# Kernel tuning notes

Measured on AMD Instinct MI355X. Metric: run time of the kernel, lower is better.

Reference implementation:

```python
import jax, jax.numpy as jnp
import numpy as np

B, H, W, C, M1, M2, NL = 16, 41, 40, 48, 12, 12, 4
EPS = 1e-5
TX = jnp.linspace(0.0, 2.0 * np.pi, H, dtype=jnp.float32)      # theta grid, len 41
TY = jnp.linspace(0.0, 15.0, W, dtype=jnp.float32)             # z grid, len 40
DTX = 2.0 * np.pi / (H - 1)
DTY = 15.0 / (W - 1)
LAM1 = (2j * np.pi) * jnp.fft.fftfreq(H, d=DTX).astype(jnp.float32)  # [H] complex64
LAM2 = (2j * np.pi) * jnp.fft.fftfreq(W, d=DTY).astype(jnp.float32)  # [W] complex64


def setup_inputs() -> dict:
    key = jax.random.key(0)
    k = jax.random.split(key, 10)
    scale = 1.0 / (C * C)
    u = lambda kk, s: scale * jax.random.uniform(kk, s, dtype=jnp.float32)
    n = lambda kk, s, sc: sc * jax.random.normal(kk, s, dtype=jnp.float32)
    return {
        "x": n(k[0], (B, H, W, 1), 1.0),
        "fc0_w": n(k[1], (C, 3), 0.3), "fc0_b": jnp.zeros((C,), jnp.float32),
        "poles1": u(k[2], (NL, C, C, M1, 2)),          # real/imag split of cfloat params
        "poles2": u(k[3], (NL, C, C, M2, 2)),
        "residues": u(k[4], (NL, C, C, M1, M2, 2)),
        "conv_w": n(k[5], (NL, C, C), 1.0 / np.sqrt(C)), "conv_b": jnp.zeros((NL, C), jnp.float32),
        "fc1_w": n(k[6], (128, C), 1.0 / np.sqrt(C)), "fc1_b": jnp.zeros((128,), jnp.float32),
        "fc2_w": n(k[7], (2, 128), 1.0 / np.sqrt(128)), "fc2_b": jnp.zeros((2,), jnp.float32),
    }


def _cplx(a):
    return a[..., 0] + 1j * a[..., 1]


def _inorm(h):  # InstanceNorm2d(affine=False): per-(b,c) over H,W, biased var
    m = h.mean(axis=(-2, -1), keepdims=True)
    v = h.var(axis=(-2, -1), keepdims=True)
    return (h - m) / jnp.sqrt(v + EPS)


def _pr2d(h, p1ri, p2ri, resri):
    # h: [B,C,H,W] real. Pole-residue Laplace spectral operator (PR2d.forward).
    p1 = _cplx(p1ri)     # [Ci,Co,M1]
    p2 = _cplx(p2ri)     # [Ci,Co,M2]
    res = _cplx(resri)   # [Ci,Co,M1,M2]
    alpha = jnp.fft.fft2(h, axes=(-2, -1))                      # [B,Ci,H,W] complex
    inv1 = 1.0 / (LAM1[None, None, None, :] - p1[..., None])    # [Ci,Co,M1,H]
    inv2 = 1.0 / (LAM2[None, None, None, :] - p2[..., None])    # [Ci,Co,M2,W]
    # output_residue1[b,k,o,x] = sum_{i,p,q} alpha * res * inv1 * inv2
    S = jnp.einsum('ikpq,ikpo,ikqx->ikox', res, inv1, inv2)     # [Ci,Co,H,W]
    res1 = jnp.einsum('biox,ikox->bkox', alpha, S)              # [B,Co,H,W]
    # output_residue2[b,k,p,q] = sum_{i,o,x} alpha * res * inv1 * inv2
    A = jnp.einsum('biox,ikpo->bikpx', alpha, inv1)             # [B,Ci,Co,M1,W]
    G = jnp.einsum('bikpx,ikqx->bikpq', A, inv2)                # [B,Ci,Co,M1,M2]
    r2 = jnp.einsum('bikpq,ikpq->bkpq', G, res)                 # [B,Co,M1,M2]
    x1 = jnp.fft.ifft2(res1, axes=(-2, -1)).real
    # reconstruction: exp(pole * t) outer products (term1/term2/term3 in torch)
    E1 = jnp.exp(p1[..., None] * TX[None, None, None, :])       # [Ci,Co,M1,H]
    E2 = jnp.exp(p2[..., None] * TY[None, None, None, :])       # [Ci,Co,M2,W]
    U = jnp.einsum('kbpq,bipz->kbiqz', r2, E1)                  # [B,Ci,Co,M2,H]
    x2 = jnp.einsum('kbiqz,biqx->kizx', U, E2).real / (H * W)   # [B,Co,H,W]
    return x1 + x2


def reference(x, fc0_w, fc0_b, poles1, poles2, residues, conv_w, conv_b,
              fc1_w, fc1_b, fc2_w, fc2_b):
    b = x.shape[0]
    gx = jnp.broadcast_to(jnp.linspace(0.0, 1.0, H, dtype=jnp.float32)[None, :, None, None], (b, H, W, 1))
    gy = jnp.broadcast_to(jnp.linspace(0.0, 1.0, W, dtype=jnp.float32)[None, None, :, None], (b, H, W, 1))
    h = jnp.concatenate([x, gx, gy], axis=-1)                   # [B,H,W,3]
    h = jnp.einsum('bhwi,ci->bhwc', h, fc0_w) + fc0_b           # fc0
    h = jnp.transpose(h, (0, 3, 1, 2))                          # [B,C,H,W]
    for l in range(NL):
        x1 = _inorm(_pr2d(_inorm(h), poles1[l], poles2[l], residues[l]))
        x2 = jnp.einsum('oi,bihw->bohw', conv_w[l], h) + conv_b[l][None, :, None, None]
        h = jnp.sin(x1 + x2)
    h = jnp.transpose(h, (0, 2, 3, 1))                          # [B,H,W,C]
    h = jnp.sin(jnp.einsum('bhwc,oc->bhwo', h, fc1_w) + fc1_b)
    out = jnp.einsum('bhwc,oc->bhwo', h, fc2_w) + fc2_b         # [B,H,W,2]
    return out
```

## Files before the change

kernel.cpp:

```cpp
#include <hip/hip_runtime.h>
#include <math.h>

#define DI __device__ __forceinline__

constexpr int B = 16, H = 41, W = 40, C = 48, M1 = 12, M2 = 12, NL = 4;
constexpr int HW = H * W;
constexpr float EPS = 1e-5f;
constexpr float PI_F = 3.14159265358979323846f;

__device__ float  g_h[2][B * C * HW];
__device__ float2 g_alpha[B * C * HW];
__device__ float2 g_inv1t[NL][C * C][H * 16];
__device__ float2 g_inv2a[NL][C * C][M2 * W];
__device__ float2 g_E1a[NL][C * C][M1 * H];
__device__ float2 g_E2a[NL][C * C][M2 * W];
__device__ float2 g_Sa[NL][C * C][HW];
__device__ float2 g_res1[B * C * HW];
__device__ float  g_x1[B * C * HW];
__device__ float2 g_r2[B * C * M1 * M2];
__device__ float2 g_Zr[C * C][B * M1 * M2];
__device__ float  g_xpart[3][B * C][HW];
__device__ float  g_mu[B * C];
__device__ float  g_rstd[B * C];
__device__ float2 g_wfh[H * H];
__device__ float2 g_wfw[W * W];

DI float2 cmadd(float2 a, float2 b, float2 acc) {
    acc.x = fmaf(a.x, b.x, fmaf(-a.y, b.y, acc.x));
    acc.y = fmaf(a.x, b.y, fmaf(a.y, b.x, acc.y));
    return acc;
}
DI float2 cmul(float2 a, float2 b) {
    return make_float2(a.x * b.x - a.y * b.y, a.x * b.y + a.y * b.x);
}

__global__ void k_tw() {
    int tid = blockIdx.x * 256 + threadIdx.x;
    if (tid < H * H) {
        int o = tid / H, h = tid % H;
        float ph = -2.0f * PI_F * (float)((o * h) % H) / (float)H;
        float s, c; sincosf(ph, &s, &c);
        g_wfh[tid] = make_float2(c, s);
    }
    int t2 = tid - H * H;
    if (t2 >= 0 && t2 < W * W) {
        int o = t2 / W, w = t2 % W;
        float ph = -2.0f * PI_F * (float)((o * w) % W) / (float)W;
        float s, c; sincosf(ph, &s, &c);
        g_wfw[t2] = make_float2(c, s);
    }
}

__global__ void k_fc0(const float* __restrict__ x, const float* __restrict__ w,
                      const float* __restrict__ bias) {
    int idx = blockIdx.x * 256 + threadIdx.x;
    if (idx >= B * C * HW) return;
    int hw = idx % HW; int bc = idx / HW; int c = bc % C; int b = bc / C;
    int hh = hw / W, ww = hw % W;
    float xv = x[b * HW + hw];
    float gx = hh * (1.0f / (H - 1));
    float gy = ww * (1.0f / (W - 1));
    g_h[0][idx] = fmaf(w[c * 3 + 0], xv, fmaf(w[c * 3 + 1], gx, fmaf(w[c * 3 + 2], gy, bias[c])));
}

__global__ __launch_bounds__(256) void k_fft(int src) {
    int bid = blockIdx.x;
    const float* hp = &g_h[src][(size_t)bid * HW];
    __shared__ float sh[HW];
    __shared__ float2 st[HW];
    __shared__ float2 swf[H * H];
    __shared__ float red[8];
    int tid = threadIdx.x;
    float s = 0.f, ss = 0.f;
    for (int i = tid; i < HW; i += 256) { float v = hp[i]; sh[i] = v; s += v; ss += v * v; }
    for (int i = tid; i < H * H; i += 256) swf[i] = g_wfh[i];
    for (int off = 32; off; off >>= 1) { s += __shfl_down(s, off); ss += __shfl_down(ss, off); }
    if ((tid & 63) == 0) { red[tid >> 6] = s; red[4 + (tid >> 6)] = ss; }
    __syncthreads();
    if (tid == 0) {
        float S = red[0] + red[1] + red[2] + red[3];
        float SS = red[4] + red[5] + red[6] + red[7];
        float mean = S * (1.0f / HW);
        float var = SS * (1.0f / HW) - mean * mean;
        red[0] = mean; red[1] = rsqrtf(var + EPS);
    }
    __syncthreads();
    float mean = red[0], rstd = red[1];
    for (int i = tid; i < HW; i += 256) sh[i] = (sh[i] - mean) * rstd;
    __syncthreads();
    for (int i = tid; i < 21 * W; i += 256) {
        int o0 = (i / W) * 2, w = i % W;
        bool pair = (o0 + 1) < H;
        float2 a0 = make_float2(0.f, 0.f), a1 = make_float2(0.f, 0.f);
        for (int h = 0; h < H; h++) {
            float v = sh[h * W + w];
            float2 t0 = swf[o0 * H + h];
            a0.x = fmaf(t0.x, v, a0.x); a0.y = fmaf(t0.y, v, a0.y);
            if (pair) {
                float2 t1 = swf[o0 * H + H + h];
                a1.x = fmaf(t1.x, v, a1.x); a1.y = fmaf(t1.y, v, a1.y);
            }
        }
        st[o0 * W + w] = a0;
        if (pair) st[(o0 + 1) * W + w] = a1;
    }
    __syncthreads();
    for (int t = tid; t < W * W; t += 256) {
        int x = t / W, w = t % W;
        swf[x * 41 + w] = g_wfw[t];
    }
    __syncthreads();
    float2* ap = &g_alpha[(size_t)bid * HW];
    for (int i = tid; i < H * 20; i += 256) {
        int o = i / 20, x0 = (i % 20) * 2;
        float2 a0 = make_float2(0.f, 0.f), a1 = make_float2(0.f, 0.f);
        for (int w = 0; w < W; w++) {
            float2 sv = st[o * W + w];
            a0 = cmadd(sv, swf[x0 * 41 + w], a0);
            a1 = cmadd(sv, swf[(x0 + 1) * 41 + w], a1);
        }
        ap[o * W + x0] = a0;
        ap[o * W + x0 + 1] = a1;
    }
}

__global__ __launch_bounds__(256) void k_tbS(const float* __restrict__ p1, const float* __restrict__ p2,
                                             const float* __restrict__ res_in) {
    int gb = blockIdx.x;
    int l = gb / (C * C), pk = gb % (C * C);
    int tid = threadIdx.x;
    __shared__ float2 sinv1[M1 * H];
    __shared__ float2 sinv2[M2 * W];
    __shared__ float2 sT[M1 * W];
    __shared__ float2 sres[M1 * M2];
    const float* pp1 = p1 + (size_t)gb * M1 * 2;
    const float* pp2 = p2 + (size_t)gb * M2 * 2;
    for (int t = tid; t < M1 * H; t += 256) {
        int p = t / H, o = t % H;
        float pr = pp1[p * 2], pi = pp1[p * 2 + 1];
        int ko = (o <= H / 2) ? o : o - H;
        float lam = (40.0f / 41.0f) * (float)ko;
        float a = -pr, b = lam - pi;
        float d = 1.0f / (a * a + b * b);
        float2 inv = make_float2(a * d, -b * d);
        sinv1[t] = inv;
        float tt = o * (2.0f * PI_F / (H - 1));
        float er = expf(pr * tt);
        float sn, cs; sincosf(pi * tt, &sn, &cs);
        g_E1a[l][pk][t] = make_float2(er * cs, er * sn);
    }
    for (int t = tid; t < M2 * W; t += 256) {
        int q = t / W, x = t % W;
        float pr = pp2[q * 2], pi = pp2[q * 2 + 1];
        int kx = (x < W / 2) ? x : x - W;
        float lam = (2.0f * PI_F * 39.0f / 600.0f) * (float)kx;
        float a = -pr, b = lam - pi;
        float d = 1.0f / (a * a + b * b);
        float2 inv = make_float2(a * d, -b * d);
        sinv2[t] = inv;
        g_inv2a[l][pk][t] = inv;
        float tt = x * (15.0f / (W - 1));
        float er = expf(pr * tt);
        float sn, cs; sincosf(pi * tt, &sn, &cs);
        g_E2a[l][pk][t] = make_float2(er * cs, er * sn);
    }
    const float2* rp = (const float2*)res_in + (size_t)gb * M1 * M2;
    for (int t = tid; t < M1 * M2; t += 256) sres[t] = rp[t];
    __syncthreads();
    for (int t = tid; t < H * 16; t += 256) {
        int o = t >> 4, p = t & 15;
        g_inv1t[l][pk][t] = (p < M1) ? sinv1[p * H + o] : make_float2(0.f, 0.f);
    }
    for (int t = tid; t < M1 * W; t += 256) {
        int p = t / W, x = t % W;
        float2 acc = make_float2(0.f, 0.f);
        for (int q = 0; q < M2; q++) acc = cmadd(sres[p * M2 + q], sinv2[q * W + x], acc);
        sT[t] = acc;
    }
    __syncthreads();
    float2* sp = g_Sa[l][pk];
    for (int t = tid; t < HW; t += 256) {
        int o = t / W, x = t % W;
        float2 acc = make_float2(0.f, 0.f);
        for (int p = 0; p < M1; p++) acc = cmadd(sinv1[p * H + o], sT[p * W + x], acc);
        sp[t] = acc;
    }
}

__global__ __launch_bounds__(256) void k_res1(int l) {
    int bid = blockIdx.x;
    int ch = bid % 7;
    int rest = bid / 7;
    int kq = rest % 12, bp = rest / 12;
    int hw = ch * 256 + threadIdx.x;
    if (hw >= HW) return;
    int b0 = bp * 2, k0 = kq * 4;
    float2 acc[2][4];
#pragma unroll
    for (int u = 0; u < 2; u++)
#pragma unroll
        for (int v = 0; v < 4; v++) acc[u][v] = make_float2(0.f, 0.f);
    for (int i = 0; i < C; i++) {
        float2 a0 = g_alpha[(size_t)((b0    ) * C + i) * HW + hw];
        float2 a1 = g_alpha[(size_t)((b0 + 1) * C + i) * HW + hw];
        float2 s0 = g_Sa[l][i * C + k0][hw];
        float2 s1 = g_Sa[l][i * C + k0 + 1][hw];
        float2 s2 = g_Sa[l][i * C + k0 + 2][hw];
        float2 s3 = g_Sa[l][i * C + k0 + 3][hw];
        acc[0][0] = cmadd(a0, s0, acc[0][0]);
        acc[0][1] = cmadd(a0, s1, acc[0][1]);
        acc[0][2] = cmadd(a0, s2, acc[0][2]);
        acc[0][3] = cmadd(a0, s3, acc[0][3]);
        acc[1][0] = cmadd(a1, s0, acc[1][0]);
        acc[1][1] = cmadd(a1, s1, acc[1][1]);
        acc[1][2] = cmadd(a1, s2, acc[1][2]);
        acc[1][3] = cmadd(a1, s3, acc[1][3]);
    }
#pragma unroll
    for (int u = 0; u < 2; u++)
#pragma unroll
        for (int v = 0; v < 4; v++)
            g_res1[(size_t)((b0 + u) * C + k0 + v) * HW + hw] = acc[u][v];
}

__global__ __launch_bounds__(256) void k_ifftfin() {
    int bid = blockIdx.x; int tid = threadIdx.x;
    __shared__ float2 s0[HW], s1[HW];
    __shared__ float2 swf[H * H];
    __shared__ float red[8];
    const float2* rp = &g_res1[(size_t)bid * HW];
    for (int i = tid; i < HW; i += 256) s0[i] = rp[i];
    for (int i = tid; i < H * H; i += 256) swf[i] = g_wfh[i];
    __syncthreads();
    for (int i = tid; i < 21 * W; i += 256) {
        int h0 = (i / W) * 2, x = i % W;
        bool pair = (h0 + 1) < H;
        float2 a0 = make_float2(0.f, 0.f), a1 = make_float2(0.f, 0.f);
        for (int o = 0; o < H; o++) {
            float2 v = s0[o * W + x];
            float2 t0 = swf[o * H + h0];
            a0.x = fmaf(v.x, t0.x, fmaf(v.y, t0.y, a0.x));
            a0.y = fmaf(v.y, t0.x, fmaf(-v.x, t0.y, a0.y));
            if (pair) {
                float2 t1 = swf[o * H + h0 + 1];
                a1.x = fmaf(v.x, t1.x, fmaf(v.y, t1.y, a1.x));
                a1.y = fmaf(v.y, t1.x, fmaf(-v.x, t1.y, a1.y));
            }
        }
        s1[h0 * W + x] = a0;
        if (pair) s1[(h0 + 1) * W + x] = a1;
    }
    __syncthreads();
    for (int t = tid; t < W * W; t += 256) {
        int x = t / W, w = t % W;
        swf[x * 41 + w] = g_wfw[t];
    }
    __syncthreads();
    float* xp = &g_x1[(size_t)bid * HW];
    const float* q0p = &g_xpart[0][bid][0];
    const float* q1p = &g_xpart[1][bid][0];
    const float* q2p = &g_xpart[2][bid][0];
    float s = 0.f, ss = 0.f;
    for (int i = tid; i < H * 20; i += 256) {
        int h = i / 20, w0 = (i % 20) * 2;
        float a0 = 0.f, a1 = 0.f;
        for (int x = 0; x < W; x++) {
            float2 v = s1[h * W + x];
            float2 t0 = swf[x * 41 + w0];
            float2 t1 = swf[x * 41 + w0 + 1];
            a0 = fmaf(v.x, t0.x, fmaf(v.y, t0.y, a0));
            a1 = fmaf(v.x, t1.x, fmaf(v.y, t1.y, a1));
        }
        int id0 = h * W + w0;
        float v0 = (a0 + q0p[id0] + q1p[id0] + q2p[id0]) * (1.0f / (H * W));
        float v1 = (a1 + q0p[id0 + 1] + q1p[id0 + 1] + q2p[id0 + 1]) * (1.0f / (H * W));
        xp[id0] = v0; xp[id0 + 1] = v1;
        s += v0 + v1; ss += v0 * v0 + v1 * v1;
    }
    for (int off = 32; off; off >>= 1) { s += __shfl_down(s, off); ss += __shfl_down(ss, off); }
    if ((tid & 63) == 0) { red[tid >> 6] = s; red[4 + (tid >> 6)] = ss; }
    __syncthreads();
    if (tid == 0) {
        float S = red[0] + red[1] + red[2] + red[3];
        float SS = red[4] + red[5] + red[6] + red[7];
        float mean = S * (1.0f / HW);
        float var = SS * (1.0f / HW) - mean * mean;
        g_mu[bid] = mean; g_rstd[bid] = rsqrtf(var + EPS);
    }
}

__global__ __launch_bounds__(320) void k_r2a(const float* __restrict__ res_in, int l) {
    int bid = blockIdx.x;
    int xcd = bid & 7, idx = bid >> 3;
    int i = (idx / (C * 4)) * 8 + xcd;
    int rem = idx % (C * 4);
    int k = rem >> 2;
    int bc = rem & 3;
    int pk = i * C + k;
    int tid = threadIdx.x;
    __shared__ float2 sY[4 * M1 * 41];
    __shared__ float2 si1t[H * 16];
    __shared__ float2 si2[M2 * 41];
    __shared__ float2 sres[M1 * M2];
    for (int t = tid; t < H * 16; t += 320) si1t[t] = g_inv1t[l][pk][t];
    for (int t = tid; t < M2 * W; t += 320) {
        int q = t / W, x = t % W;
        si2[q * 41 + x] = g_inv2a[l][pk][t];
    }
    const float2* rp = (const float2*)res_in + (size_t)(l * C * C + pk) * M1 * M2;
    for (int t = tid; t < M1 * M2; t += 320) sres[t] = rp[t];
    __syncthreads();
    {
        int ph = tid / 160;
        int r2t = tid % 160;
        int bloc = r2t / 40, x = r2t % 40;
        int b = bc * 4 + bloc;
        int p0 = ph * 6;
        const float2* ap = &g_alpha[(size_t)(b * C + i) * HW + x];
        float2 yacc[6];
#pragma unroll
        for (int p = 0; p < 6; p++) yacc[p] = make_float2(0.f, 0.f);
        for (int o = 0; o < H; o++) {
            float2 a = ap[o * W];
            const float4* e4 = (const float4*)&si1t[o * 16 + p0];
#pragma unroll
            for (int j = 0; j < 3; j++) {
                float4 ee = e4[j];
                yacc[2 * j]     = cmadd(make_float2(ee.x, ee.y), a, yacc[2 * j]);
                yacc[2 * j + 1] = cmadd(make_float2(ee.z, ee.w), a, yacc[2 * j + 1]);
            }
        }
#pragma unroll
        for (int p = 0; p < 6; p++) sY[(bloc * M1 + p0 + p) * 41 + x] = yacc[p];
    }
    __syncthreads();
    if (tid < 288) {
        int bloc = tid / 72, rem2 = tid % 72;
        int p = rem2 / 6, qh = rem2 % 6;
        int q0 = qh * 2;
        float2 zacc0 = make_float2(0.f, 0.f), zacc1 = make_float2(0.f, 0.f);
        const float2* yrow = &sY[(bloc * M1 + p) * 41];
        const float2* s2a = &si2[q0 * 41];
        const float2* s2b = &si2[(q0 + 1) * 41];
        for (int x = 0; x < W; x++) {
            float2 y = yrow[x];
            zacc0 = cmadd(y, s2a[x], zacc0);
            zacc1 = cmadd(y, s2b[x], zacc1);
        }
        int b = bc * 4 + bloc;
        float2* out = &g_Zr[pk][b * (M1 * M2) + p * M2 + q0];
        out[0] = cmul(sres[p * M2 + q0], zacc0);
        out[1] = cmul(sres[p * M2 + q0 + 1], zacc1);
    }
}

__global__ __launch_bounds__(256) void k_r2b() {
    int t = blockIdx.x * 256 + threadIdx.x;
    if (t >= B * C * M1 * M2) return;
    int pq = t % (M1 * M2);
    int k = (t / (M1 * M2)) % C;
    int b = t / (M1 * M2 * C);
    float2 acc = make_float2(0.f, 0.f);
    for (int i = 0; i < C; i++) {
        float2 v = g_Zr[i * C + k][b * (M1 * M2) + pq];
        acc.x += v.x; acc.y += v.y;
    }
    g_r2[(size_t)(b * C + k) * (M1 * M2) + pq] = acc;
}

constexpr int XNCI = 2;
__global__ __launch_bounds__(256) void k_x2p(int l) {
    int bid = blockIdx.x;
    int xcd = bid & 7, rest = bid >> 3;
    int part = rest % 3;
    int idx = rest / 3;
    int k = (idx / B) * 8 + xcd;
    int b = idx % B;
    int tid = threadIdx.x;
    __shared__ float2 sE1[XNCI * M1 * 44];
    __shared__ float2 sV [XNCI * M1 * 40];
    __shared__ float2 sE2[XNCI * M2 * 41];
    __shared__ float2 sr2[XNCI * M1 * M2];
    int xh = tid % 20, zq = tid / 20;
    int x0 = xh * 2, z0 = zq * 4;
    float accr[4][2];
#pragma unroll
    for (int zi = 0; zi < 4; zi++) { accr[zi][0] = 0.f; accr[zi][1] = 0.f; }

    int cg0 = part * (C / XNCI / 3);
    for (int cg = cg0; cg < cg0 + C / XNCI / 3; cg++) {
        for (int t = tid; t < XNCI * M1 * 44; t += 256) {
            int j = t / (M1 * 44), rem = t % (M1 * 44);
            int p = rem / 44, z = rem % 44;
            sE1[t] = (z < H) ? g_E1a[l][(cg * XNCI + j) * C + k][p * H + z]
                             : make_float2(0.f, 0.f);
        }
        for (int t = tid; t < XNCI * M2 * W; t += 256) {
            int j = t / (M2 * W), rem = t % (M2 * W);
            sE2[(t / W) * 41 + (t % W)] = g_E2a[l][(cg * XNCI + j) * C + k][rem];
        }
        for (int t = tid; t < XNCI * M1 * M2; t += 256) {
            int j = t / (M1 * M2);
            sr2[t] = g_r2[(size_t)(b * C + cg * XNCI + j) * (M1 * M2) + (t % (M1 * M2))];
        }
        __syncthreads();
        for (int r = 0; r < 2; r++) {
            int id = tid + r * 256;
            if (id < XNCI * 6 * W) {
                int j = id / (6 * W), rem = id % (6 * W);
                int pp = rem / W, x = rem % W;
                int p0 = pp * 2;
                float2 a0 = make_float2(0.f, 0.f), a1 = make_float2(0.f, 0.f);
#pragma unroll
                for (int q = 0; q < M2; q++) {
                    float2 e = sE2[(j * M2 + q) * 41 + x];
                    a0 = cmadd(sr2[j * (M1 * M2) + p0 * M2 + q], e, a0);
                    a1 = cmadd(sr2[j * (M1 * M2) + (p0 + 1) * M2 + q], e, a1);
                }
                sV[(j * M1 + p0) * 40 + x] = a0;
                sV[(j * M1 + p0 + 1) * 40 + x] = a1;
            }
        }
        __syncthreads();
        if (tid < 240 && z0 < H) {
            for (int jp = 0; jp < XNCI * M1; jp++) {
                float4 v  = *(const float4*)&sV[jp * 40 + x0];
                float4 eA = *(const float4*)&sE1[jp * 44 + z0];
                float4 eB = *(const float4*)&sE1[jp * 44 + z0 + 2];
                accr[0][0] = fmaf(eA.x, v.x, fmaf(-eA.y, v.y, accr[0][0]));
                accr[0][1] = fmaf(eA.x, v.z, fmaf(-eA.y, v.w, accr[0][1]));
                accr[1][0] = fmaf(eA.z, v.x, fmaf(-eA.w, v.y, accr[1][0]));
                accr[1][1] = fmaf(eA.z, v.z, fmaf(-eA.w, v.w, accr[1][1]));
                accr[2][0] = fmaf(eB.x, v.x, fmaf(-eB.y, v.y, accr[2][0]));
                accr[2][1] = fmaf(eB.x, v.z, fmaf(-eB.y, v.w, accr[2][1]));
                accr[3][0] = fmaf(eB.z, v.x, fmaf(-eB.w, v.y, accr[3][0]));
                accr[3][1] = fmaf(eB.z, v.z, fmaf(-eB.w, v.w, accr[3][1]));
            }
        }
        __syncthreads();
    }
    float* op = &g_xpart[part][b * C + k][0];
    if (tid < 240 && z0 < H) {
#pragma unroll
        for (int zi = 0; zi < 4; zi++) {
            int z = z0 + zi;
            if (z < H) { op[z * W + x0] = accr[zi][0]; op[z * W + x0 + 1] = accr[zi][1]; }
        }
    }
}

constexpr int TILE = 128;
constexpr int NTILE = (HW + TILE - 1) / TILE;
__global__ __launch_bounds__(256) void k_comb(const float* __restrict__ cw,
                                              const float* __restrict__ cb, int l, int src) {
    int b = blockIdx.x / NTILE;
    int t0 = (blockIdx.x % NTILE) * TILE;
    int tid = threadIdx.x;
    __shared__ float shh[C * TILE];
    __shared__ float scw[C * C];
    __shared__ float smu[C], srs[C], scb[C];
    for (int i = tid; i < C * C; i += 256) scw[i] = cw[l * C * C + i];
    for (int i = tid; i < C; i += 256) {
        smu[i] = g_mu[b * C + i]; srs[i] = g_rstd[b * C + i]; scb[i] = cb[l * C + i];
    }
    for (int i = tid; i < C * TILE; i += 256) {
        int c = i / TILE, t = i % TILE; int hw = t0 + t;
        shh[i] = (hw < HW) ? g_h[src][(size_t)(b * C + c) * HW + hw] : 0.f;
    }
    __syncthreads();
    for (int i = tid; i < C * TILE; i += 256) {
        int o = i / TILE, t = i % TILE; int hw = t0 + t;
        if (hw >= HW) continue;
        float acc = scb[o];
        for (int ci = 0; ci < C; ci++) acc = fmaf(scw[o * C + ci], shh[ci * TILE + t], acc);
        float prn = (g_x1[(size_t)(b * C + o) * HW + hw] - smu[o]) * srs[o];
        g_h[src ^ 1][(size_t)(b * C + o) * HW + hw] = sinf(prn + acc);
    }
}

__global__ __launch_bounds__(256) void k_head(const float* __restrict__ w1, const float* __restrict__ b1,
                                              const float* __restrict__ w2, const float* __restrict__ b2,
                                              float* __restrict__ out, int src) {
    __shared__ float sw1[128 * C];
    __shared__ float sb1[128], sw2[2 * 128];
    int tid = threadIdx.x;
    for (int i = tid; i < 128 * C; i += 256) sw1[i] = w1[i];
    for (int i = tid; i < 128; i += 256) sb1[i] = b1[i];
    for (int i = tid; i < 256; i += 256) sw2[i] = w2[i];
    __syncthreads();
    int pt = blockIdx.x * 256 + tid;
    if (pt >= B * HW) return;
    int b = pt / HW, hw = pt % HW;
    float hv[C];
#pragma unroll
    for (int c = 0; c < C; c++) hv[c] = g_h[src][(size_t)(b * C + c) * HW + hw];
    float o0 = b2[0], o1 = b2[1];
    for (int j = 0; j < 128; j++) {
        float a = sb1[j];
#pragma unroll
        for (int c = 0; c < C; c++) a = fmaf(sw1[j * C + c], hv[c], a);
        float sv = sinf(a);
        o0 = fmaf(sw2[j], sv, o0);
        o1 = fmaf(sw2[128 + j], sv, o1);
    }
    out[pt * 2 + 0] = o0; out[pt * 2 + 1] = o1;
}

extern "C" void kernel_launch(void* const* d_in, const int* in_sizes, int n_in,
                              void* d_out, int out_size, void* d_ws, size_t ws_size,
                              hipStream_t stream) {
    const float* x    = (const float*)d_in[0];
    const float* fc0w = (const float*)d_in[1];
    const float* fc0b = (const float*)d_in[2];
    const float* p1   = (const float*)d_in[3];
    const float* p2   = (const float*)d_in[4];
    const float* res  = (const float*)d_in[5];
    const float* cw   = (const float*)d_in[6];
    const float* cb   = (const float*)d_in[7];
    const float* w1   = (const float*)d_in[8];
    const float* b1   = (const float*)d_in[9];
    const float* w2   = (const float*)d_in[10];
    const float* b2   = (const float*)d_in[11];
    float* out = (float*)d_out;

    k_tw<<<(H * H + W * W + 255) / 256, 256, 0, stream>>>();
    k_fc0<<<(B * C * HW + 255) / 256, 256, 0, stream>>>(x, fc0w, fc0b);
    k_tbS<<<NL * C * C, 256, 0, stream>>>(p1, p2, res);
    int src = 0;
    for (int l = 0; l < NL; l++) {
        k_fft<<<B * C, 256, 0, stream>>>(src);
        k_res1<<<672, 256, 0, stream>>>(l);
        k_r2a<<<C * C * 4, 320, 0, stream>>>(res, l);
        k_r2b<<<(B * C * M1 * M2 + 255) / 256, 256, 0, stream>>>();
        k_x2p<<<3 * B * C, 256, 0, stream>>>(l);
        k_ifftfin<<<B * C, 256, 0, stream>>>();
        k_comb<<<B * NTILE, 256, 0, stream>>>(cw, cb, l, src);
        src ^= 1;
    }
    k_head<<<(B * HW + 255) / 256, 256, 0, stream>>>(w1, b1, w2, b2, out, src);
}
```

Baseline: 1.779 ms.

## Register-block FFT and inverse-FFT DFT loops and split x2p over six parts

The DFT matmul loops in the forward FFT and the inverse-FFT/finalise kernels now have each thread compute a 2x4 output tile, using float4 shared-memory loads and reusing each twiddle and data value across several accumulators. The twiddle stride is padded to 42 so the vector loads stay aligned. Separately, the x2p channel reduction is split six ways instead of three, which doubles the block count and the number of partial buffers summed in the finalise step. This cuts shared-memory traffic and adds parallelism, at the cost of only 210 of 256 threads being active in those loops and extra partial-sum memory traffic.

Result: faster. 1.696 ms (-4.7%).

```diff
diff --git a/kernel.cpp b/kernel.cpp
--- a/kernel.cpp
+++ b/kernel.cpp
@@ -5,6 +5,7 @@
 
 constexpr int B = 16, H = 41, W = 40, C = 48, M1 = 12, M2 = 12, NL = 4;
 constexpr int HW = H * W;
+constexpr int NPART = 6;
 constexpr float EPS = 1e-5f;
 constexpr float PI_F = 3.14159265358979323846f;
 
@@ -19,7 +20,7 @@
 __device__ float  g_x1[B * C * HW];
 __device__ float2 g_r2[B * C * M1 * M2];
 __device__ float2 g_Zr[C * C][B * M1 * M2];
-__device__ float  g_xpart[3][B * C][HW];
+__device__ float  g_xpart[NPART][B * C][HW];
 __device__ float  g_mu[B * C];
 __device__ float  g_rstd[B * C];
 __device__ float2 g_wfh[H * H];
@@ -66,9 +67,9 @@
 __global__ __launch_bounds__(256) void k_fft(int src) {
     int bid = blockIdx.x;
     const float* hp = &g_h[src][(size_t)bid * HW];
-    __shared__ float sh[HW];
-    __shared__ float2 st[HW];
-    __shared__ float2 swf[H * H];
+    __shared__ __align__(16) float sh[HW];
+    __shared__ __align__(16) float2 st[HW];
+    __shared__ __align__(16) float2 swf[H * H];
     __shared__ float red[8];
     int tid = threadIdx.x;
     float s = 0.f, ss = 0.f;
@@ -88,21 +89,33 @@
     float mean = red[0], rstd = red[1];
     for (int i = tid; i < HW; i += 256) sh[i] = (sh[i] - mean) * rstd;
     __syncthreads();
-    for (int i = tid; i < 21 * W; i += 256) {
-        int o0 = (i / W) * 2, w = i % W;
+    if (tid < 210) {
+        int op = tid / 10, wq = tid % 10;
+        int o0 = op * 2, w0 = wq * 4;
         bool pair = (o0 + 1) < H;
-        float2 a0 = make_float2(0.f, 0.f), a1 = make_float2(0.f, 0.f);
+        int o1 = pair ? o0 + 1 : o0;
+        float2 a0[4], a1[4];
+#pragma unroll
+        for (int j = 0; j < 4; j++) { a0[j] = make_float2(0.f, 0.f); a1[j] = make_float2(0.f, 0.f); }
         for (int h = 0; h < H; h++) {
-            float v = sh[h * W + w];
+            float4 v = *(const float4*)&sh[h * W + w0];
             float2 t0 = swf[o0 * H + h];
-            a0.x = fmaf(t0.x, v, a0.x); a0.y = fmaf(t0.y, v, a0.y);
-            if (pair) {
-                float2 t1 = swf[o0 * H + H + h];
-                a1.x = fmaf(t1.x, v, a1.x); a1.y = fmaf(t1.y, v, a1.y);
-            }
-        }
-        st[o0 * W + w] = a0;
-        if (pair) st[(o0 + 1) * W + w] = a1;
+            float2 t1 = swf[o1 * H + h];
+            a0[0].x = fmaf(t0.x, v.x, a0[0].x); a0[0].y = fmaf(t0.y, v.x, a0[0].y);
+            a0[1].x = fmaf(t0.x, v.y, a0[1].x); a0[1].y = fmaf(t0.y, v.y, a0[1].y);
+            a0[2].x = fmaf(t0.x, v.z, a0[2].x); a0[2].y = fmaf(t0.y, v.z, a0[2].y);
+            a0[3].x = fmaf(t0.x, v.w, a0[3].x); a0[3].y = fmaf(t0.y, v.w, a0[3].y);
+            a1[0].x = fmaf(t1.x, v.x, a1[0].x); a1[0].y = fmaf(t1.y, v.x, a1[0].y);
+            a1[1].x = fmaf(t1.x, v.y, a1[1].x); a1[1].y = fmaf(t1.y, v.y, a1[1].y);
+            a1[2].x = fmaf(t1.x, v.z, a1[2].x); a1[2].y = fmaf(t1.y, v.z, a1[2].y);
+            a1[3].x = fmaf(t1.x, v.w, a1[3].x); a1[3].y = fmaf(t1.y, v.w, a1[3].y);
+        }
+#pragma unroll
+        for (int j = 0; j < 4; j++) st[o0 * W + w0 + j] = a0[j];
+        if (pair) {
+#pragma unroll
+            for (int j = 0; j < 4; j++) st[o1 * W + w0 + j] = a1[j];
+        }
     }
     __syncthreads();
     for (int t = tid; t < W * W; t += 256) {
@@ -111,16 +124,30 @@
     }
     __syncthreads();
     float2* ap = &g_alpha[(size_t)bid * HW];
-    for (int i = tid; i < H * 20; i += 256) {
-        int o = i / 20, x0 = (i % 20) * 2;
-        float2 a0 = make_float2(0.f, 0.f), a1 = make_float2(0.f, 0.f);
+    if (tid < 210) {
+        int op = tid / 10, xq = tid % 10;
+        int o0 = op * 2, x0 = xq * 4;
+        bool pair = (o0 + 1) < H;
+        int o1 = pair ? o0 + 1 : o0;
+        float2 c0[4], c1[4];
+#pragma unroll
+        for (int j = 0; j < 4; j++) { c0[j] = make_float2(0.f, 0.f); c1[j] = make_float2(0.f, 0.f); }
         for (int w = 0; w < W; w++) {
-            float2 sv = st[o * W + w];
-            a0 = cmadd(sv, swf[x0 * 41 + w], a0);
-            a1 = cmadd(sv, swf[(x0 + 1) * 41 + w], a1);
-        }
-        ap[o * W + x0] = a0;
-        ap[o * W + x0 + 1] = a1;
+            float2 s0v = st[o0 * W + w];
+            float2 s1v = st[o1 * W + w];
+#pragma unroll
+            for (int j = 0; j < 4; j++) {
+                float2 e = swf[(x0 + j) * 41 + w];
+                c0[j] = cmadd(s0v, e, c0[j]);
+                c1[j] = cmadd(s1v, e, c1[j]);
+            }
+        }
+#pragma unroll
+        for (int j = 0; j < 4; j++) ap[o0 * W + x0 + j] = c0[j];
+        if (pair) {
+#pragma unroll
+            for (int j = 0; j < 4; j++) ap[o1 * W + x0 + j] = c1[j];
+        }
     }
 }
 
@@ -225,57 +252,110 @@
 
 __global__ __launch_bounds__(256) void k_ifftfin() {
     int bid = blockIdx.x; int tid = threadIdx.x;
-    __shared__ float2 s0[HW], s1[HW];
-    __shared__ float2 swf[H * H];
+    __shared__ __align__(16) float2 s0[HW], s1[HW];
+    __shared__ __align__(16) float2 swf[H * H];
     __shared__ float red[8];
     const float2* rp = &g_res1[(size_t)bid * HW];
     for (int i = tid; i < HW; i += 256) s0[i] = rp[i];
     for (int i = tid; i < H * H; i += 256) swf[i] = g_wfh[i];
     __syncthreads();
-    for (int i = tid; i < 21 * W; i += 256) {
-        int h0 = (i / W) * 2, x = i % W;
+    if (tid < 210) {
+        int hp = tid / 10, xq = tid % 10;
+        int h0 = hp * 2, x0 = xq * 4;
         bool pair = (h0 + 1) < H;
-        float2 a0 = make_float2(0.f, 0.f), a1 = make_float2(0.f, 0.f);
+        int h1 = pair ? h0 + 1 : h0;
+        float2 a0[4], a1[4];
+#pragma unroll
+        for (int j = 0; j < 4; j++) { a0[j] = make_float2(0.f, 0.f); a1[j] = make_float2(0.f, 0.f); }
         for (int o = 0; o < H; o++) {
-            float2 v = s0[o * W + x];
+            float4 v01 = *(const float4*)&s0[o * W + x0];
+            float4 v23 = *(const float4*)&s0[o * W + x0 + 2];
             float2 t0 = swf[o * H + h0];
-            a0.x = fmaf(v.x, t0.x, fmaf(v.y, t0.y, a0.x));
-            a0.y = fmaf(v.y, t0.x, fmaf(-v.x, t0.y, a0.y));
-            if (pair) {
-                float2 t1 = swf[o * H + h0 + 1];
-                a1.x = fmaf(v.x, t1.x, fmaf(v.y, t1.y, a1.x));
-                a1.y = fmaf(v.y, t1.x, fmaf(-v.x, t1.y, a1.y));
-            }
-        }
-        s1[h0 * W + x] = a0;
-        if (pair) s1[(h0 + 1) * W + x] = a1;
+            float2 t1 = swf[o * H + h1];
+            a0[0].x = fmaf(v01.x, t0.x, fmaf(v01.y, t0.y, a0[0].x));
+            a0[0].y = fmaf(v01.y, t0.x, fmaf(-v01.x, t0.y, a0[0].y));
+            a0[1].x = fmaf(v01.z, t0.x, fmaf(v01.w, t0.y, a0[1].x));
+            a0[1].y = fmaf(v01.w, t0.x, fmaf(-v01.z, t0.y, a0[1].y));
+            a0[2].x = fmaf(v23.x, t0.x, fmaf(v23.y, t0.y, a0[2].x));
+            a0[2].y = fmaf(v23.y, t0.x, fmaf(-v23.x, t0.y, a0[2].y));
+            a0[3].x = fmaf(v23.z, t0.x, fmaf(v23.w, t0.y, a0[3].x));
+            a0[3].y = fmaf(v23.w, t0.x, fmaf(-v23.z, t0.y, a0[3].y));
+            a1[0].x = fmaf(v01.x, t1.x, fmaf(v01.y, t1.y, a1[0].x));
+            a1[0].y = fmaf(v01.y, t1.x, fmaf(-v01.x, t1.y, a1[0].y));
+            a1[1].x = fmaf(v01.z, t1.x, fmaf(v01.w, t1.y, a1[1].x));
+            a1[1].y = fmaf(v01.w, t1.x, fmaf(-v01.z, t1.y, a1[1].y));
+            a1[2].x = fmaf(v23.x, t1.x, fmaf(v23.y, t1.y, a1[2].x));
+            a1[2].y = fmaf(v23.y, t1.x, fmaf(-v23.x, t1.y, a1[2].y));
+            a1[3].x = fmaf(v23.z, t1.x, fmaf(v23.w, t1.y, a1[3].x));
+            a1[3].y = fmaf(v23.w, t1.x, fmaf(-v23.z, t1.y, a1[3].y));
+        }
+#pragma unroll
+        for (int j = 0; j < 4; j++) s1[h0 * W + x0 + j] = a0[j];
+        if (pair) {
+#pragma unroll
+            for (int j = 0; j < 4; j++) s1[h1 * W + x0 + j] = a1[j];
+        }
     }
     __syncthreads();
     for (int t = tid; t < W * W; t += 256) {
         int x = t / W, w = t % W;
-        swf[x * 41 + w] = g_wfw[t];
+        swf[x * 42 + w] = g_wfw[t];
     }
     __syncthreads();
     float* xp = &g_x1[(size_t)bid * HW];
-    const float* q0p = &g_xpart[0][bid][0];
-    const float* q1p = &g_xpart[1][bid][0];
-    const float* q2p = &g_xpart[2][bid][0];
     float s = 0.f, ss = 0.f;
-    for (int i = tid; i < H * 20; i += 256) {
-        int h = i / 20, w0 = (i % 20) * 2;
-        float a0 = 0.f, a1 = 0.f;
+    if (tid < 210) {
+        int hp = tid / 10, wq = tid % 10;
+        int h0 = hp * 2, w0 = wq * 4;
+        bool pair = (h0 + 1) < H;
+        int h1 = pair ? h0 + 1 : h0;
+        float acc0[4] = {0.f, 0.f, 0.f, 0.f}, acc1[4] = {0.f, 0.f, 0.f, 0.f};
         for (int x = 0; x < W; x++) {
-            float2 v = s1[h * W + x];
-            float2 t0 = swf[x * 41 + w0];
-            float2 t1 = swf[x * 41 + w0 + 1];
-            a0 = fmaf(v.x, t0.x, fmaf(v.y, t0.y, a0));
-            a1 = fmaf(v.x, t1.x, fmaf(v.y, t1.y, a1));
-        }
-        int id0 = h * W + w0;
-        float v0 = (a0 + q0p[id0] + q1p[id0] + q2p[id0]) * (1.0f / (H * W));
-        float v1 = (a1 + q0p[id0 + 1] + q1p[id0 + 1] + q2p[id0 + 1]) * (1.0f / (H * W));
-        xp[id0] = v0; xp[id0 + 1] = v1;
-        s += v0 + v1; ss += v0 * v0 + v1 * v1;
+            float2 u0 = s1[h0 * W + x];
+            float2 u1 = s1[h1 * W + x];
+            float4 e01 = *(const float4*)&swf[x * 42 + w0];
+            float4 e23 = *(const float4*)&swf[x * 42 + w0 + 2];
+            acc0[0] = fmaf(u0.x, e01.x, fmaf(u0.y, e01.y, acc0[0]));
+            acc0[1] = fmaf(u0.x, e01.z, fmaf(u0.y, e01.w, acc0[1]));
+            acc0[2] = fmaf(u0.x, e23.x, fmaf(u0.y, e23.y, acc0[2]));
+            acc0[3] = fmaf(u0.x, e23.z, fmaf(u0.y, e23.w, acc0[3]));
+            acc1[0] = fmaf(u1.x, e01.x, fmaf(u1.y, e01.y, acc1[0]));
+            acc1[1] = fmaf(u1.x, e01.z, fmaf(u1.y, e01.w, acc1[1]));
+            acc1[2] = fmaf(u1.x, e23.x, fmaf(u1.y, e23.y, acc1[2]));
+            acc1[3] = fmaf(u1.x, e23.z, fmaf(u1.y, e23.w, acc1[3]));
+        }
+        {
+            int base = h0 * W + w0;
+            float4 q0 = *(const float4*)&g_xpart[0][bid][base];
+            float4 q1 = *(const float4*)&g_xpart[1][bid][base];
+            float4 q2 = *(const float4*)&g_xpart[2][bid][base];
+            float4 q3 = *(const float4*)&g_xpart[3][bid][base];
+            float4 q4 = *(const float4*)&g_xpart[4][bid][base];
+            float4 q5 = *(const float4*)&g_xpart[5][bid][base];
+            float vv[4];
+            vv[0] = (acc0[0] + q0.x + q1.x + q2.x + q3.x + q4.x + q5.x) * (1.0f / (H * W));
+            vv[1] = (acc0[1] + q0.y + q1.y + q2.y + q3.y + q4.y + q5.y) * (1.0f / (H * W));
+            vv[2] = (acc0[2] + q0.z + q1.z + q2.z + q3.z + q4.z + q5.z) * (1.0f / (H * W));
+            vv[3] = (acc0[3] + q0.w + q1.w + q2.w + q3.w + q4.w + q5.w) * (1.0f / (H * W));
+#pragma unroll
+            for (int j = 0; j < 4; j++) { xp[base + j] = vv[j]; s += vv[j]; ss += vv[j] * vv[j]; }
+        }
+        if (pair) {
+            int base = h1 * W + w0;
+            float4 q0 = *(const float4*)&g_xpart[0][bid][base];
+            float4 q1 = *(const float4*)&g_xpart[1][bid][base];
+            float4 q2 = *(const float4*)&g_xpart[2][bid][base];
+            float4 q3 = *(const float4*)&g_xpart[3][bid][base];
+            float4 q4 = *(const float4*)&g_xpart[4][bid][base];
+            float4 q5 = *(const float4*)&g_xpart[5][bid][base];
+            float vv[4];
+            vv[0] = (acc1[0] + q0.x + q1.x + q2.x + q3.x + q4.x + q5.x) * (1.0f / (H * W));
+            vv[1] = (acc1[1] + q0.y + q1.y + q2.y + q3.y + q4.y + q5.y) * (1.0f / (H * W));
+            vv[2] = (acc1[2] + q0.z + q1.z + q2.z + q3.z + q4.z + q5.z) * (1.0f / (H * W));
+            vv[3] = (acc1[3] + q0.w + q1.w + q2.w + q3.w + q4.w + q5.w) * (1.0f / (H * W));
+#pragma unroll
+            for (int j = 0; j < 4; j++) { xp[base + j] = vv[j]; s += vv[j]; ss += vv[j] * vv[j]; }
+        }
     }
     for (int off = 32; off; off >>= 1) { s += __shfl_down(s, off); ss += __shfl_down(ss, off); }
     if ((tid & 63) == 0) { red[tid >> 6] = s; red[4 + (tid >> 6)] = ss; }
@@ -372,8 +452,8 @@
 __global__ __launch_bounds__(256) void k_x2p(int l) {
     int bid = blockIdx.x;
     int xcd = bid & 7, rest = bid >> 3;
-    int part = rest % 3;
-    int idx = rest / 3;
+    int part = rest % NPART;
+    int idx = rest / NPART;
     int k = (idx / B) * 8 + xcd;
     int b = idx % B;
     int tid = threadIdx.x;
@@ -387,8 +467,8 @@
 #pragma unroll
     for (int zi = 0; zi < 4; zi++) { accr[zi][0] = 0.f; accr[zi][1] = 0.f; }
 
-    int cg0 = part * (C / XNCI / 3);
-    for (int cg = cg0; cg < cg0 + C / XNCI / 3; cg++) {
+    int cg0 = part * (C / XNCI / NPART);
+    for (int cg = cg0; cg < cg0 + C / XNCI / NPART; cg++) {
         for (int t = tid; t < XNCI * M1 * 44; t += 256) {
             int j = t / (M1 * 44), rem = t % (M1 * 44);
             int p = rem / 44, z = rem % 44;
@@ -532,7 +612,7 @@
         k_res1<<<672, 256, 0, stream>>>(l);
         k_r2a<<<C * C * 4, 320, 0, stream>>>(res, l);
         k_r2b<<<(B * C * M1 * M2 + 255) / 256, 256, 0, stream>>>();
-        k_x2p<<<3 * B * C, 256, 0, stream>>>(l);
+        k_x2p<<<NPART * B * C, 256, 0, stream>>>(l);
         k_ifftfin<<<B * C, 256, 0, stream>>>();
         k_comb<<<B * NTILE, 256, 0, stream>>>(cw, cb, l, src);
         src ^= 1;
```
